# Optimization experiments

Measured on AMD Instinct MI355X. Metric: run time of the kernel, lower is better.

Reference implementation:

```python
import jax, jax.numpy as jnp
import numpy as np

DIM = 512
HIDDEN = 1024  # 2.0 * dim
QK = 128
MAX_PEAKS = 256
LN_EPS = 1e-5


def setup_inputs() -> dict:
    key = jax.random.key(0)
    ks = jax.random.split(key, 10)
    b, n = 8, 2048
    x = jax.random.normal(ks[0], (b, n, DIM), dtype=jnp.float32)
    moverz_sin = jax.random.normal(ks[1], (b, n, QK // 2), dtype=jnp.float32)
    moverz_cos = jax.random.normal(ks[2], (b, n, QK // 2), dtype=jnp.float32)
    src_key_padding_mask = jax.random.randint(ks[3], (b, 1, n), 0, 2) > 0
    ln_w = jnp.ones((DIM,), jnp.float32)
    ln_b = jnp.zeros((DIM,), jnp.float32)
    W_hid = jax.random.normal(ks[4], (DIM, 2 * HIDDEN + QK), dtype=jnp.float32) * 0.02
    b_hid = jnp.zeros((2 * HIDDEN + QK,), jnp.float32)
    gamma = jax.random.normal(ks[5], (2, QK), dtype=jnp.float32) * 0.02
    beta = jnp.zeros((2, QK), jnp.float32)
    W_out = jax.random.normal(ks[6], (HIDDEN, DIM), dtype=jnp.float32) * 0.02
    b_out = jnp.zeros((DIM,), jnp.float32)
    return dict(x=x, moverz_sin=moverz_sin, moverz_cos=moverz_cos,
                src_key_padding_mask=src_key_padding_mask,
                ln_w=ln_w, ln_b=ln_b, W_hid=W_hid, b_hid=b_hid,
                gamma=gamma, beta=beta, W_out=W_out, b_out=b_out)


def _apply_moverz(x, sin, cos):
    x0, x1 = x[..., 0::2], x[..., 1::2]
    return jnp.concatenate([x0 * cos - x1 * sin, x1 * cos + x0 * sin], axis=-1)


def reference(x, moverz_sin, moverz_cos, src_key_padding_mask,
              ln_w, ln_b, W_hid, b_hid, gamma, beta, W_out, b_out):
    # LayerNorm + Linear + SiLU
    mu = jnp.mean(x, axis=-1, keepdims=True)
    var = jnp.mean(jnp.square(x - mu), axis=-1, keepdims=True)
    xn = (x - mu) * jax.lax.rsqrt(var + LN_EPS) * ln_w + ln_b
    uv_base = jax.nn.silu(xn @ W_hid + b_hid)  # [b,n,2H+QK]
    u = uv_base[..., :HIDDEN]
    v = uv_base[..., HIDDEN:2 * HIDDEN]
    base = uv_base[..., 2 * HIDDEN:]
    # OffsetScale (heads=2) -> q, k
    q = base * gamma[0] + beta[0]
    k = base * gamma[1] + beta[1]
    q = _apply_moverz(q, moverz_sin, moverz_cos)
    k = _apply_moverz(k, moverz_sin, moverz_cos)
    qk = jnp.einsum('bnr,bmr->bnm', q, k)
    qk = jnp.where(src_key_padding_mask, 0.0, qk)
    attn = jnp.square(jax.nn.relu(qk)) / (MAX_PEAKS * QK)
    out = jnp.einsum('bnm,bmd->bnd', attn, v) * u
    return out @ W_out + b_out + x
```

## Files before the change

### kernel.cpp

```cpp
#include <hip/hip_runtime.h>
#include <hip/hip_bf16.h>
#include <hip/hip_fp8.h>

typedef short short8 __attribute__((ext_vector_type(8)));
typedef float floatx4 __attribute__((ext_vector_type(4)));
typedef int intx8 __attribute__((ext_vector_type(8)));

constexpr int BATCH = 8, SEQ = 2048, DIMC = 512, HID = 1024, QKD = 128, NHID = 2176;
constexpr int TOK = BATCH * SEQ;

constexpr size_t OFF_XN8 = 0;
constexpr size_t OFF_WH8 = OFF_XN8 + (size_t)TOK * DIMC;
constexpr size_t OFF_WO8 = OFF_WH8 + (size_t)NHID * DIMC;
constexpr size_t OFF_U8  = OFF_WO8 + (size_t)DIMC * HID;
constexpr size_t OFF_V8  = OFF_U8  + (size_t)TOK * HID;
constexpr size_t OFF_BSE = OFF_V8  + (size_t)TOK * HID;
constexpr size_t OFF_Q8  = OFF_BSE + (size_t)TOK * QKD * 2;
constexpr size_t OFF_K8C = OFF_Q8  + (size_t)TOK * QKD;
constexpr size_t OFF_VT8 = OFF_K8C + (size_t)TOK * QKD;
constexpr size_t OFF_P8  = OFF_VT8 + (size_t)BATCH * HID * SEQ;
constexpr size_t OFF_HU8 = OFF_P8  + (size_t)BATCH * SEQ * SEQ;
constexpr size_t OFF_CPS = OFF_HU8 + (size_t)TOK * HID;
constexpr size_t OFF_IPS = OFF_CPS + (size_t)TOK * 4;
constexpr size_t OFF_NTL = OFF_IPS + (size_t)TOK * 4;

__device__ inline void gload_lds16(const void* g, void* l) {
    __builtin_amdgcn_global_load_lds(
        (const __attribute__((address_space(1))) void*)g,
        (__attribute__((address_space(3))) void*)l, 16, 0, 0);
}

#if __has_builtin(__builtin_amdgcn_cvt_pk_fp8_f32)
__device__ inline int cvtpk8(float a, float b) {
    return __builtin_amdgcn_cvt_pk_fp8_f32(a, b, 0, false);
}
__device__ inline unsigned char f2fp8(float v) {
    return (unsigned char)(cvtpk8(v, v) & 0xff);
}
#else
__device__ inline unsigned char f2fp8(float v) {
    __hip_fp8_e4m3 t(v); return t.__x;
}
__device__ inline int cvtpk8(float a, float b) {
    return (int)f2fp8(a) | ((int)f2fp8(b) << 8);
}
#endif
#if __has_builtin(__builtin_amdgcn_cvt_f32_fp8)
__device__ inline float fp82f(unsigned char b) {
    return __builtin_amdgcn_cvt_f32_fp8((int)b, 0);
}
#else
__device__ inline float fp82f(unsigned char b) {
    __hip_fp8_e4m3 t; t.__x = b; return (float)t;
}
#endif
__device__ inline float fast_rcp(float x) { return __builtin_amdgcn_rcpf(x); }
__device__ inline float fast_silu(float v) { return v * fast_rcp(1.0f + __expf(-v)); }

__global__ __launch_bounds__(256) void scan_kernel(const int* __restrict__ mask,
                                                   int* __restrict__ cpos,
                                                   int* __restrict__ ipos,
                                                   int* __restrict__ ntl,
                                                   unsigned char* __restrict__ k8c) {
    int b = blockIdx.x;
    __shared__ int sh[256];
    __shared__ int base;
    if (threadIdx.x == 0) base = 0;
    __syncthreads();
    for (int c = 0; c < 8; c++) {
        int n = c * 256 + threadIdx.x;
        int um = (mask[(size_t)b * SEQ + n] == 0) ? 1 : 0;
        sh[threadIdx.x] = um;
        __syncthreads();
        for (int off = 1; off < 256; off <<= 1) {
            int v = (threadIdx.x >= off) ? sh[threadIdx.x - off] : 0;
            __syncthreads();
            sh[threadIdx.x] += v;
            __syncthreads();
        }
        int incl = sh[threadIdx.x];
        int cp = um ? (base + incl - 1) : -1;
        cpos[(size_t)b * SEQ + n] = cp;
        if (cp >= 0) ipos[(size_t)b * SEQ + cp] = n;
        __syncthreads();
        if (threadIdx.x == 255) base += incl;
        __syncthreads();
    }
    int cnt = base;
    int nt = (cnt + 127) >> 7;
    if (threadIdx.x == 0) ntl[b] = nt;
    for (int c = cnt + threadIdx.x; c < SEQ; c += 256)
        ipos[(size_t)b * SEQ + c] = 0;
    uint4 z = {0, 0, 0, 0};
    for (int r = cnt + threadIdx.x; r < nt * 128; r += 256) {
        uint4* p = (uint4*)&k8c[((size_t)b * SEQ + r) * QKD];
        #pragma unroll
        for (int j = 0; j < 8; j++) p[j] = z;
    }
}

__global__ __launch_bounds__(256) void ln_kernel(const float* __restrict__ x,
                                                 const float* __restrict__ w,
                                                 const float* __restrict__ b,
                                                 unsigned char* __restrict__ xn8) {
    int t = blockIdx.x;
    const float* xr = x + (size_t)t * DIMC;
    float2 v = ((const float2*)xr)[threadIdx.x];
    float s = v.x + v.y;
    float ss = v.x * v.x + v.y * v.y;
    for (int o = 32; o; o >>= 1) { s += __shfl_down(s, o); ss += __shfl_down(ss, o); }
    __shared__ float red[8];
    int wid = threadIdx.x >> 6, lane = threadIdx.x & 63;
    if (lane == 0) { red[wid] = s; red[4 + wid] = ss; }
    __syncthreads();
    if (threadIdx.x == 0) {
        float a = red[0] + red[1] + red[2] + red[3];
        float q = red[4] + red[5] + red[6] + red[7];
        float mu = a * (1.0f / DIMC);
        red[0] = mu;
        red[4] = q * (1.0f / DIMC) - mu * mu;
    }
    __syncthreads();
    float mu = red[0];
    float inv = rsqrtf(red[4] + 1e-5f);
    int c = threadIdx.x * 2;
    float y0 = (v.x - mu) * inv * w[c] + b[c];
    float y1 = (v.y - mu) * inv * w[c + 1] + b[c + 1];
    int p = cvtpk8(y0, y1);
    uchar2 o2; o2.x = (unsigned char)p; o2.y = (unsigned char)(p >> 8);
    *(uchar2*)&xn8[(size_t)t * DIMC + c] = o2;
}

__global__ __launch_bounds__(256) void cvt_kernel(const float* __restrict__ Wh,
                                                  const float* __restrict__ Wo,
                                                  unsigned char* __restrict__ WhT8,
                                                  unsigned char* __restrict__ WoT8) {
    int i = blockIdx.x * 256 + threadIdx.x;
    const int total1 = NHID * DIMC;
    const int total2 = DIMC * HID;
    if (i < total1) {
        int n = i / DIMC, k = i % DIMC;
        WhT8[i] = f2fp8(Wh[(size_t)k * NHID + n]);
    } else if (i < total1 + total2) {
        int j = i - total1;
        int d = j / HID, h = j % HID;
        WoT8[j] = f2fp8(Wo[(size_t)h * DIMC + d] * 64.0f);
    }
}

__global__ __launch_bounds__(256) void qkrot_kernel(const __hip_bfloat16* __restrict__ bse,
                                                    const float* __restrict__ sn,
                                                    const float* __restrict__ cs,
                                                    const int* __restrict__ cpos,
                                                    const float* __restrict__ gamma,
                                                    const float* __restrict__ beta,
                                                    unsigned char* __restrict__ q8,
                                                    unsigned char* __restrict__ k8c) {
    int t = blockIdx.x * 4 + (threadIdx.x >> 6);
    int j = threadIdx.x & 63;
    const __hip_bfloat16* base = bse + (size_t)t * QKD;
    float b0 = __bfloat162float(base[2 * j]);
    float b1 = __bfloat162float(base[2 * j + 1]);
    float q0 = b0 * gamma[2 * j] + beta[2 * j];
    float q1 = b1 * gamma[2 * j + 1] + beta[2 * j + 1];
    float k0 = b0 * gamma[QKD + 2 * j] + beta[QKD + 2 * j];
    float k1 = b1 * gamma[QKD + 2 * j + 1] + beta[QKD + 2 * j + 1];
    float s = sn[(size_t)t * 64 + j];
    float c = cs[(size_t)t * 64 + j];
    int pq = cvtpk8((q0 * c - q1 * s) * 16.f, (q1 * c + q0 * s) * 16.f);
    q8[(size_t)t * QKD + j]      = (unsigned char)pq;
    q8[(size_t)t * QKD + 64 + j] = (unsigned char)(pq >> 8);
    int cp = cpos[t];
    if (cp >= 0) {
        int bb = t >> 11;
        int pk = cvtpk8((k0 * c - k1 * s) * 16.f, (k1 * c + k0 * s) * 16.f);
        size_t kr = ((size_t)bb * SEQ + cp) * QKD;
        k8c[kr + j]      = (unsigned char)pk;
        k8c[kr + 64 + j] = (unsigned char)(pk >> 8);
    }
}

__global__ __launch_bounds__(256) void vtc_kernel(const unsigned char* __restrict__ v8,
                                                  const int* __restrict__ ipos,
                                                  const int* __restrict__ ntl,
                                                  unsigned char* __restrict__ Vt8) {
    int b = blockIdx.z;
    int c0 = blockIdx.x * 64, h0 = blockIdx.y * 64;
    if (c0 >= (ntl[b] << 7)) return;
    __shared__ unsigned char tile[64][68];
    int r = threadIdx.x >> 4;
    int c4 = (threadIdx.x & 15) << 2;
    #pragma unroll
    for (int i = 0; i < 4; i++) {
        int rr = i * 16 + r;
        int src = ipos[(size_t)b * SEQ + c0 + rr];
        *(uchar4*)&tile[rr][c4] = *(const uchar4*)&v8[((size_t)b * SEQ + src) * HID + h0 + c4];
    }
    __syncthreads();
    #pragma unroll
    for (int i = 0; i < 4; i++) {
        int hh = i * 16 + r;
        uchar4 o;
        o.x = tile[c4][hh]; o.y = tile[c4 + 1][hh]; o.z = tile[c4 + 2][hh]; o.w = tile[c4 + 3][hh];
        *(uchar4*)&Vt8[((size_t)b * HID + h0 + hh) * SEQ + c0 + c4] = o;
    }
}

template <int EPI, int RAS>
__global__ __launch_bounds__(256, 4) void gemm_mx(
    const unsigned char* __restrict__ A, int lda, long long sA,
    const unsigned char* __restrict__ Bt, int ldb, long long sB,
    int K,
    const float* __restrict__ bias,
    const unsigned char* __restrict__ U8, int ldu, long long sU,
    const float* __restrict__ Xres, int ldx,
    float oscale,
    unsigned char* __restrict__ C8, int ldc8, long long sC8,
    unsigned char* __restrict__ V8out,
    __hip_bfloat16* __restrict__ Cbse,
    float* __restrict__ Cf, int ldcf,
    const int* __restrict__ ntl) {
    __shared__ unsigned char As[128 * 128];
    __shared__ unsigned char Bs[128 * 128];

    int m0, n0;
    if (RAS == 0) {
        int lin = blockIdx.x + gridDim.x * blockIdx.y;
        int xcd = lin & 7, j = lin >> 3;
        int gy = gridDim.y;
        m0 = (xcd * (gridDim.x >> 3) + j / gy) * 128;
        n0 = (j % gy) * 128;
    } else {
        int fid = blockIdx.x + gridDim.x * (blockIdx.y + gridDim.y * blockIdx.z);
        int b = fid & 7;
        int r = fid >> 3;
        int gy = gridDim.y;
        n0 = (r % gy) * 128;
        m0 = (r / gy) * 128;
        A += (size_t)b * sA;
        Bt += (size_t)b * sB;
        if (C8) C8 += (size_t)b * sC8;
        if (U8) U8 += (size_t)b * sU;
        if (EPI == 1 && n0 >= (ntl[b] << 7)) return;
        if (EPI == 2) K = ntl[b] << 7;
    }

    int tid = threadIdx.x, lane = tid & 63, wid = tid >> 6;
    int wr = (wid >> 1) * 64, wc = (wid & 1) * 64;
    int r16 = lane & 15, kq = lane >> 4;

    int srow = lane >> 3;
    int sc = (((lane & 7) ^ ((lane >> 3) & 7)) << 4);

    floatx4 acc[4][4] = {};
    const int SCL = 0x7F7F7F7F;

    #define FRGRD(P, row, dst) { \
        uint4* p_ = (uint4*)&(dst); \
        p_[0] = *(const uint4*)&(P)[(row) * 128 + ((((kq * 2)     ^ ((row) & 7))) << 4)]; \
        p_[1] = *(const uint4*)&(P)[(row) * 128 + ((((kq * 2 + 1) ^ ((row) & 7))) << 4)]; }

    for (int kt = 0; kt < K; kt += 128) {
        #pragma unroll
        for (int i = 0; i < 4; i++) {
            int r0 = wid * 32 + i * 8;
            gload_lds16(&A[(size_t)(m0 + r0 + srow) * lda + kt + sc], &As[r0 * 128]);
            gload_lds16(&Bt[(size_t)(n0 + r0 + srow) * ldb + kt + sc], &Bs[r0 * 128]);
        }
        __syncthreads();
        intx8 bfr[4];
        #pragma unroll
        for (int ni = 0; ni < 4; ni++) FRGRD(Bs, wc + ni * 16 + r16, bfr[ni])
        #pragma unroll
        for (int mo = 0; mo < 2; mo++) {
            intx8 afr[2];
            #pragma unroll
            for (int mi = 0; mi < 2; mi++) FRGRD(As, wr + (mo * 2 + mi) * 16 + r16, afr[mi])
            #pragma unroll
            for (int mi = 0; mi < 2; mi++)
                #pragma unroll
                for (int ni = 0; ni < 4; ni++)
                    acc[mo * 2 + mi][ni] = __builtin_amdgcn_mfma_scale_f32_16x16x128_f8f6f4(
                        afr[mi], bfr[ni], acc[mo * 2 + mi][ni], 0, 0, 0, SCL, 0, SCL);
        }
        __syncthreads();
    }
    #undef FRGRD

    #pragma unroll
    for (int mi = 0; mi < 4; mi++) {
        #pragma unroll
        for (int ni = 0; ni < 4; ni++) {
            int rbase = m0 + wr + mi * 16 + kq * 4;
            int col = n0 + wc + ni * 16 + r16;
            if (EPI == 3) {
                #pragma unroll
                for (int i = 0; i < 4; i++) {
                    float v = acc[mi][ni][i] * oscale + bias[col] + Xres[(size_t)(rbase + i) * ldx + col];
                    Cf[(size_t)(rbase + i) * ldcf + col] = v;
                }
            } else {
                float e[4];
                #pragma unroll
                for (int i = 0; i < 4; i++) {
                    float v = acc[mi][ni][i];
                    if (EPI == 0) {
                        v = fast_silu(v + bias[col]);
                    } else if (EPI == 1) {
                        v = v > 0.0f ? v * v * 16.0f : 0.0f;
                    } else {
                        v *= oscale * fp82f(U8[(size_t)(rbase + i) * ldu + col]);
                    }
                    e[i] = v;
                }
                int p01 = cvtpk8(e[0], e[1]);
                int p23 = cvtpk8(e[2], e[3]);
                unsigned char byt[4] = {
                    (unsigned char)p01, (unsigned char)(p01 >> 8),
                    (unsigned char)p23, (unsigned char)(p23 >> 8)};
                if (EPI == 0) {
                    if (n0 < 1024) {
                        #pragma unroll
                        for (int i = 0; i < 4; i++)
                            C8[(size_t)(rbase + i) * HID + col] = byt[i];
                    } else if (n0 < 2048) {
                        #pragma unroll
                        for (int i = 0; i < 4; i++)
                            V8out[(size_t)(rbase + i) * HID + col - 1024] = byt[i];
                    } else {
                        #pragma unroll
                        for (int i = 0; i < 4; i++)
                            Cbse[(size_t)(rbase + i) * QKD + col - 2048] = __float2bfloat16(e[i]);
                    }
                } else {
                    #pragma unroll
                    for (int i = 0; i < 4; i++)
                        C8[(size_t)(rbase + i) * ldc8 + col] = byt[i];
                }
            }
        }
    }
}

extern "C" void kernel_launch(void* const* d_in, const int* in_sizes, int n_in,
                              void* d_out, int out_size, void* d_ws, size_t ws_size,
                              hipStream_t stream) {
    const float* x     = (const float*)d_in[0];
    const float* msin  = (const float*)d_in[1];
    const float* mcos  = (const float*)d_in[2];
    const int*   mask  = (const int*)d_in[3];
    const float* lnw   = (const float*)d_in[4];
    const float* lnb   = (const float*)d_in[5];
    const float* Wh    = (const float*)d_in[6];
    const float* bh    = (const float*)d_in[7];
    const float* gamma = (const float*)d_in[8];
    const float* beta  = (const float*)d_in[9];
    const float* Wo    = (const float*)d_in[10];
    const float* bo    = (const float*)d_in[11];
    float* out = (float*)d_out;
    char* ws = (char*)d_ws;

    unsigned char*  xn8  = (unsigned char*)(ws + OFF_XN8);
    unsigned char*  WhT8 = (unsigned char*)(ws + OFF_WH8);
    unsigned char*  WoT8 = (unsigned char*)(ws + OFF_WO8);
    unsigned char*  u8   = (unsigned char*)(ws + OFF_U8);
    unsigned char*  v8   = (unsigned char*)(ws + OFF_V8);
    __hip_bfloat16* bse  = (__hip_bfloat16*)(ws + OFF_BSE);
    unsigned char*  q8   = (unsigned char*)(ws + OFF_Q8);
    unsigned char*  k8c  = (unsigned char*)(ws + OFF_K8C);
    unsigned char*  Vt8  = (unsigned char*)(ws + OFF_VT8);
    unsigned char*  P8   = (unsigned char*)(ws + OFF_P8);
    unsigned char*  hu8  = (unsigned char*)(ws + OFF_HU8);
    int*            cpos = (int*)(ws + OFF_CPS);
    int*            ipos = (int*)(ws + OFF_IPS);
    int*            ntl  = (int*)(ws + OFF_NTL);

    scan_kernel<<<BATCH, 256, 0, stream>>>(mask, cpos, ipos, ntl, k8c);

    ln_kernel<<<TOK, 256, 0, stream>>>(x, lnw, lnb, xn8);

    cvt_kernel<<<(NHID * DIMC + DIMC * HID + 255) / 256, 256, 0, stream>>>(Wh, Wo, WhT8, WoT8);

    gemm_mx<0, 0><<<dim3(TOK / 128, NHID / 128), 256, 0, stream>>>(
        xn8, DIMC, 0, WhT8, DIMC, 0, DIMC, bh,
        nullptr, 0, 0, nullptr, 0, 0.0f,
        u8, 0, 0, v8, bse, nullptr, 0, nullptr);

    qkrot_kernel<<<TOK / 4, 256, 0, stream>>>(bse, msin, mcos, cpos, gamma, beta, q8, k8c);

    vtc_kernel<<<dim3(SEQ / 64, HID / 64, BATCH), 256, 0, stream>>>(v8, ipos, ntl, Vt8);

    gemm_mx<1, 1><<<dim3(SEQ / 128, SEQ / 128, BATCH), 256, 0, stream>>>(
        q8, QKD, (long long)SEQ * QKD, k8c, QKD, (long long)SEQ * QKD, QKD, nullptr,
        nullptr, 0, 0, nullptr, 0, 0.0f,
        P8, SEQ, (long long)SEQ * SEQ, nullptr, nullptr, nullptr, 0, ntl);

    gemm_mx<2, 1><<<dim3(SEQ / 128, HID / 128, BATCH), 256, 0, stream>>>(
        P8, SEQ, (long long)SEQ * SEQ, Vt8, SEQ, (long long)HID * SEQ, SEQ, nullptr,
        u8, HID, (long long)SEQ * HID, nullptr, 0, 1.9073486328125e-06f ,
        hu8, HID, (long long)SEQ * HID, nullptr, nullptr, nullptr, 0, ntl);

    gemm_mx<3, 0><<<dim3(TOK / 128, DIMC / 128), 256, 0, stream>>>(
        hu8, HID, 0, WoT8, HID, 0, HID, bo,
        nullptr, 0, 0, x, DIMC, 2.384185791015625e-07f ,
        nullptr, 0, 0, nullptr, nullptr, out, DIMC, nullptr);
}
```

Measured before the change: 136.9 us.

## Merge small prep kernels and vectorize LayerNorm to one wave per row

```diff
diff --git a/kernel.cpp b/kernel.cpp
--- a/kernel.cpp
+++ b/kernel.cpp
@@ -57,11 +57,30 @@
 __device__ inline float fast_rcp(float x) { return __builtin_amdgcn_rcpf(x); }
 __device__ inline float fast_silu(float v) { return v * fast_rcp(1.0f + __expf(-v)); }
 
-__global__ __launch_bounds__(256) void scan_kernel(const int* __restrict__ mask,
+constexpr int CVT_BLOCKS = (NHID * DIMC + DIMC * HID + 255) / 256;
+__global__ __launch_bounds__(256) void prep_kernel(const int* __restrict__ mask,
                                                    int* __restrict__ cpos,
                                                    int* __restrict__ ipos,
                                                    int* __restrict__ ntl,
-                                                   unsigned char* __restrict__ k8c) {
+                                                   unsigned char* __restrict__ k8c,
+                                                   const float* __restrict__ Wh,
+                                                   const float* __restrict__ Wo,
+                                                   unsigned char* __restrict__ WhT8,
+                                                   unsigned char* __restrict__ WoT8) {
+    if (blockIdx.x >= 8) {
+        int i = (blockIdx.x - 8) * 256 + threadIdx.x;
+        const int total1 = NHID * DIMC;
+        const int total2 = DIMC * HID;
+        if (i < total1) {
+            int n = i / DIMC, k = i % DIMC;
+            WhT8[i] = f2fp8(Wh[(size_t)k * NHID + n]);
+        } else if (i < total1 + total2) {
+            int j = i - total1;
+            int d = j / HID, h = j % HID;
+            WoT8[j] = f2fp8(Wo[(size_t)h * DIMC + d] * 64.0f);
+        }
+        return;
+    }
     int b = blockIdx.x;
     __shared__ int sh[256];
     __shared__ int base;
@@ -103,89 +122,78 @@
                                                  const float* __restrict__ w,
                                                  const float* __restrict__ b,
                                                  unsigned char* __restrict__ xn8) {
-    int t = blockIdx.x;
-    const float* xr = x + (size_t)t * DIMC;
-    float2 v = ((const float2*)xr)[threadIdx.x];
-    float s = v.x + v.y;
-    float ss = v.x * v.x + v.y * v.y;
+    int t = blockIdx.x * 4 + (threadIdx.x >> 6);
+    int lane = threadIdx.x & 63;
+    const float* xr = x + (size_t)t * DIMC + lane * 8;
+    float4 v0 = *(const float4*)xr;
+    float4 v1 = *(const float4*)(xr + 4);
+    float s = v0.x + v0.y + v0.z + v0.w + v1.x + v1.y + v1.z + v1.w;
+    float ss = v0.x * v0.x + v0.y * v0.y + v0.z * v0.z + v0.w * v0.w
+             + v1.x * v1.x + v1.y * v1.y + v1.z * v1.z + v1.w * v1.w;
+    #pragma unroll
     for (int o = 32; o; o >>= 1) { s += __shfl_down(s, o); ss += __shfl_down(ss, o); }
-    __shared__ float red[8];
-    int wid = threadIdx.x >> 6, lane = threadIdx.x & 63;
-    if (lane == 0) { red[wid] = s; red[4 + wid] = ss; }
-    __syncthreads();
-    if (threadIdx.x == 0) {
-        float a = red[0] + red[1] + red[2] + red[3];
-        float q = red[4] + red[5] + red[6] + red[7];
-        float mu = a * (1.0f / DIMC);
-        red[0] = mu;
-        red[4] = q * (1.0f / DIMC) - mu * mu;
-    }
-    __syncthreads();
-    float mu = red[0];
-    float inv = rsqrtf(red[4] + 1e-5f);
-    int c = threadIdx.x * 2;
-    float y0 = (v.x - mu) * inv * w[c] + b[c];
-    float y1 = (v.y - mu) * inv * w[c + 1] + b[c + 1];
-    int p = cvtpk8(y0, y1);
-    uchar2 o2; o2.x = (unsigned char)p; o2.y = (unsigned char)(p >> 8);
-    *(uchar2*)&xn8[(size_t)t * DIMC + c] = o2;
-}
-
-__global__ __launch_bounds__(256) void cvt_kernel(const float* __restrict__ Wh,
-                                                  const float* __restrict__ Wo,
-                                                  unsigned char* __restrict__ WhT8,
-                                                  unsigned char* __restrict__ WoT8) {
-    int i = blockIdx.x * 256 + threadIdx.x;
-    const int total1 = NHID * DIMC;
-    const int total2 = DIMC * HID;
-    if (i < total1) {
-        int n = i / DIMC, k = i % DIMC;
-        WhT8[i] = f2fp8(Wh[(size_t)k * NHID + n]);
-    } else if (i < total1 + total2) {
-        int j = i - total1;
-        int d = j / HID, h = j % HID;
-        WoT8[j] = f2fp8(Wo[(size_t)h * DIMC + d] * 64.0f);
-    }
-}
-
-__global__ __launch_bounds__(256) void qkrot_kernel(const __hip_bfloat16* __restrict__ bse,
-                                                    const float* __restrict__ sn,
-                                                    const float* __restrict__ cs,
-                                                    const int* __restrict__ cpos,
-                                                    const float* __restrict__ gamma,
-                                                    const float* __restrict__ beta,
-                                                    unsigned char* __restrict__ q8,
-                                                    unsigned char* __restrict__ k8c) {
-    int t = blockIdx.x * 4 + (threadIdx.x >> 6);
-    int j = threadIdx.x & 63;
-    const __hip_bfloat16* base = bse + (size_t)t * QKD;
-    float b0 = __bfloat162float(base[2 * j]);
-    float b1 = __bfloat162float(base[2 * j + 1]);
-    float q0 = b0 * gamma[2 * j] + beta[2 * j];
-    float q1 = b1 * gamma[2 * j + 1] + beta[2 * j + 1];
-    float k0 = b0 * gamma[QKD + 2 * j] + beta[QKD + 2 * j];
-    float k1 = b1 * gamma[QKD + 2 * j + 1] + beta[QKD + 2 * j + 1];
-    float s = sn[(size_t)t * 64 + j];
-    float c = cs[(size_t)t * 64 + j];
-    int pq = cvtpk8((q0 * c - q1 * s) * 16.f, (q1 * c + q0 * s) * 16.f);
-    q8[(size_t)t * QKD + j]      = (unsigned char)pq;
-    q8[(size_t)t * QKD + 64 + j] = (unsigned char)(pq >> 8);
-    int cp = cpos[t];
-    if (cp >= 0) {
-        int bb = t >> 11;
-        int pk = cvtpk8((k0 * c - k1 * s) * 16.f, (k1 * c + k0 * s) * 16.f);
-        size_t kr = ((size_t)bb * SEQ + cp) * QKD;
-        k8c[kr + j]      = (unsigned char)pk;
-        k8c[kr + 64 + j] = (unsigned char)(pk >> 8);
-    }
-}
-
-__global__ __launch_bounds__(256) void vtc_kernel(const unsigned char* __restrict__ v8,
-                                                  const int* __restrict__ ipos,
-                                                  const int* __restrict__ ntl,
-                                                  unsigned char* __restrict__ Vt8) {
-    int b = blockIdx.z;
-    int c0 = blockIdx.x * 64, h0 = blockIdx.y * 64;
+    s = __shfl(s, 0); ss = __shfl(ss, 0);
+    float mu = s * (1.0f / DIMC);
+    float inv = rsqrtf(ss * (1.0f / DIMC) - mu * mu + 1e-5f);
+    int c = lane * 8;
+    float4 w0 = *(const float4*)&w[c], w1 = *(const float4*)&w[c + 4];
+    float4 b0 = *(const float4*)&b[c], b1 = *(const float4*)&b[c + 4];
+    float y0 = (v0.x - mu) * inv * w0.x + b0.x;
+    float y1 = (v0.y - mu) * inv * w0.y + b0.y;
+    float y2 = (v0.z - mu) * inv * w0.z + b0.z;
+    float y3 = (v0.w - mu) * inv * w0.w + b0.w;
+    float y4 = (v1.x - mu) * inv * w1.x + b1.x;
+    float y5 = (v1.y - mu) * inv * w1.y + b1.y;
+    float y6 = (v1.z - mu) * inv * w1.z + b1.z;
+    float y7 = (v1.w - mu) * inv * w1.w + b1.w;
+    int p01 = cvtpk8(y0, y1), p23 = cvtpk8(y2, y3);
+    int p45 = cvtpk8(y4, y5), p67 = cvtpk8(y6, y7);
+    uint2 o2;
+    o2.x = (unsigned)(p01 & 0xffff) | ((unsigned)(p23 & 0xffff) << 16);
+    o2.y = (unsigned)(p45 & 0xffff) | ((unsigned)(p67 & 0xffff) << 16);
+    *(uint2*)&xn8[(size_t)t * DIMC + c] = o2;
+}
+
+__global__ __launch_bounds__(256) void qv_kernel(const __hip_bfloat16* __restrict__ bse,
+                                                 const float* __restrict__ sn,
+                                                 const float* __restrict__ cs,
+                                                 const int* __restrict__ cpos,
+                                                 const float* __restrict__ gamma,
+                                                 const float* __restrict__ beta,
+                                                 unsigned char* __restrict__ q8,
+                                                 unsigned char* __restrict__ k8c,
+                                                 const unsigned char* __restrict__ v8,
+                                                 const int* __restrict__ ipos,
+                                                 const int* __restrict__ ntl,
+                                                 unsigned char* __restrict__ Vt8) {
+    if (blockIdx.x < 4096) {
+        int t = blockIdx.x * 4 + (threadIdx.x >> 6);
+        int j = threadIdx.x & 63;
+        const __hip_bfloat16* base = bse + (size_t)t * QKD;
+        float b0 = __bfloat162float(base[2 * j]);
+        float b1 = __bfloat162float(base[2 * j + 1]);
+        float q0 = b0 * gamma[2 * j] + beta[2 * j];
+        float q1 = b1 * gamma[2 * j + 1] + beta[2 * j + 1];
+        float k0 = b0 * gamma[QKD + 2 * j] + beta[QKD + 2 * j];
+        float k1 = b1 * gamma[QKD + 2 * j + 1] + beta[QKD + 2 * j + 1];
+        float s = sn[(size_t)t * 64 + j];
+        float c = cs[(size_t)t * 64 + j];
+        int pq = cvtpk8((q0 * c - q1 * s) * 16.f, (q1 * c + q0 * s) * 16.f);
+        q8[(size_t)t * QKD + j]      = (unsigned char)pq;
+        q8[(size_t)t * QKD + 64 + j] = (unsigned char)(pq >> 8);
+        int cp = cpos[t];
+        if (cp >= 0) {
+            int bb = t >> 11;
+            int pk = cvtpk8((k0 * c - k1 * s) * 16.f, (k1 * c + k0 * s) * 16.f);
+            size_t kr = ((size_t)bb * SEQ + cp) * QKD;
+            k8c[kr + j]      = (unsigned char)pk;
+            k8c[kr + 64 + j] = (unsigned char)(pk >> 8);
+        }
+        return;
+    }
+    int v = blockIdx.x - 4096;
+    int b = v >> 9;
+    int c0 = (v & 31) * 64, h0 = ((v >> 5) & 15) * 64;
     if (c0 >= (ntl[b] << 7)) return;
     __shared__ unsigned char tile[64][68];
     int r = threadIdx.x >> 4;
@@ -375,20 +383,18 @@
     int*            ipos = (int*)(ws + OFF_IPS);
     int*            ntl  = (int*)(ws + OFF_NTL);
 
-    scan_kernel<<<BATCH, 256, 0, stream>>>(mask, cpos, ipos, ntl, k8c);
-
-    ln_kernel<<<TOK, 256, 0, stream>>>(x, lnw, lnb, xn8);
-
-    cvt_kernel<<<(NHID * DIMC + DIMC * HID + 255) / 256, 256, 0, stream>>>(Wh, Wo, WhT8, WoT8);
+    prep_kernel<<<8 + CVT_BLOCKS, 256, 0, stream>>>(mask, cpos, ipos, ntl, k8c,
+                                                    Wh, Wo, WhT8, WoT8);
+
+    ln_kernel<<<TOK / 4, 256, 0, stream>>>(x, lnw, lnb, xn8);
 
     gemm_mx<0, 0><<<dim3(TOK / 128, NHID / 128), 256, 0, stream>>>(
         xn8, DIMC, 0, WhT8, DIMC, 0, DIMC, bh,
         nullptr, 0, 0, nullptr, 0, 0.0f,
         u8, 0, 0, v8, bse, nullptr, 0, nullptr);
 
-    qkrot_kernel<<<TOK / 4, 256, 0, stream>>>(bse, msin, mcos, cpos, gamma, beta, q8, k8c);
-
-    vtc_kernel<<<dim3(SEQ / 64, HID / 64, BATCH), 256, 0, stream>>>(v8, ipos, ntl, Vt8);
+    qv_kernel<<<8192, 256, 0, stream>>>(bse, msin, mcos, cpos, gamma, beta,
+                                        q8, k8c, v8, ipos, ntl, Vt8);
 
     gemm_mx<1, 1><<<dim3(SEQ / 128, SEQ / 128, BATCH), 256, 0, stream>>>(
         q8, QKD, (long long)SEQ * QKD, k8c, QKD, (long long)SEQ * QKD, QKD, nullptr,
```

Measured after the change: 120.8 us. -11.7%, faster.
